# Kernel optimization log

Hardware: AMD Instinct MI355X
Metric: run time of the kernel (lower is better)

The kernel has to match this reference:

```python
import jax, jax.numpy as jnp
import numpy as np

S = 7
BB = 2          # boxes per cell
C = 20          # classes
L_COORD = 5.0
L_NOOBJ = 0.5
L_OBJ = 1.0
L_CLASS = 1.0
BATCH = 8192


def setup_inputs() -> dict:
    key = jax.random.key(0)
    k1, k2, k3, k4 = jax.random.split(key, 4)
    pred = jax.random.normal(k1, (BATCH, S, S, BB * 5 + C), dtype=jnp.float32)
    cls = jax.random.uniform(k2, (BATCH, S, S, C), dtype=jnp.float32)
    # obj conf must be exactly 1.0 where an object exists (obj_mask test is ==1)
    conf = (jax.random.uniform(k3, (BATCH, S, S, 1)) < 0.3).astype(jnp.float32)
    box = jax.random.uniform(k4, (BATCH, S, S, 4), dtype=jnp.float32)  # cx,cy,w,h in [0,1)
    target = jnp.concatenate([cls, conf, box], axis=-1)
    return {"pred": pred, "target": target}


def _iou(a, b):
    # a: (..., BB, 4) cx,cy,w,h ; b: (..., 1, 4)  -> iou (..., BB)
    ax1, ay1 = a[..., 0] - a[..., 2] / 2, a[..., 1] - a[..., 3] / 2
    ax2, ay2 = a[..., 0] + a[..., 2] / 2, a[..., 1] + a[..., 3] / 2
    bx1, by1 = b[..., 0] - b[..., 2] / 2, b[..., 1] - b[..., 3] / 2
    bx2, by2 = b[..., 0] + b[..., 2] / 2, b[..., 1] + b[..., 3] / 2
    iw = jnp.clip(jnp.minimum(ax2, bx2) - jnp.maximum(ax1, bx1), 0.0)
    ih = jnp.clip(jnp.minimum(ay2, by2) - jnp.maximum(ay1, by1), 0.0)
    inter = iw * ih
    union = jnp.abs(a[..., 2] * a[..., 3]) + jnp.abs(b[..., 2] * b[..., 3]) - inter
    return inter / (union + 1e-6)


def reference(pred, target):
    # pred: (N,S,S,B*5+C), target: (N,S,S,5+C)
    objf = (target[..., C] == 1.0).astype(pred.dtype)        # (N,S,S)
    noobjf = 1.0 - objf
    pred_boxes = pred[..., C:].reshape(-1, S, S, BB, 5)       # (N,S,S,B,5) [conf,cx,cy,w,h]
    tb = target[..., C:]                                      # (N,S,S,5)

    ious = _iou(pred_boxes[..., 1:], tb[..., None, 1:])       # (N,S,S,B)
    best = jnp.argmax(ious, axis=-1)                          # responsible box index
    iou_best = jnp.max(ious, axis=-1)                         # (N,S,S)
    pb = jnp.take_along_axis(pred_boxes, best[..., None, None], axis=3)[..., 0, :]  # (N,S,S,5)

    center = jnp.sum((tb[..., 1:3] - pb[..., 1:3]) ** 2, axis=-1)
    # pred wh: pow(2).sqrt().sqrt() == sqrt(|wh|)
    wh = jnp.sum((jnp.sqrt(tb[..., 3:]) - jnp.sqrt(jnp.abs(pb[..., 3:]))) ** 2, axis=-1)
    conf_sq = (tb[..., 0] - pb[..., 0]) ** 2
    cls_sq = jnp.sum((pred[..., :C] - target[..., :C]) ** 2, axis=-1)

    loss = jnp.sum(
        objf * (L_COORD * (center + wh) + L_OBJ * conf_sq + L_CLASS * cls_sq)
        + noobjf * L_NOOBJ * conf_sq
    )
    avg_iou = jnp.sum(iou_best * objf) / jnp.maximum(jnp.sum(objf), 1.0)
    return loss, avg_iou
```

## Files before the change

### kernel.cpp

```cpp
#include <hip/hip_runtime.h>

#define S 7
#define BB 2
#define CLS 20
#define NCELLS (8192 * S * S)
#define CPB 64
#define THREADS 64
#define NBLK (NCELLS / CPB)
#define PRED_F 30
#define TGT_F 25

#define PRED_Q (CPB * PRED_F / 4)
#define TGT_Q  (CPB * TGT_F / 4)

__device__ __forceinline__ float iou_fn(float ax, float ay, float aw, float ah,
                                        float bx, float by, float bw, float bh) {
    float ax1 = ax - aw * 0.5f, ay1 = ay - ah * 0.5f;
    float ax2 = ax + aw * 0.5f, ay2 = ay + ah * 0.5f;
    float bx1 = bx - bw * 0.5f, by1 = by - bh * 0.5f;
    float bx2 = bx + bw * 0.5f, by2 = by + bh * 0.5f;
    float iw = fmaxf(fminf(ax2, bx2) - fmaxf(ax1, bx1), 0.0f);
    float ih = fmaxf(fminf(ay2, by2) - fmaxf(ay1, by1), 0.0f);
    float inter = iw * ih;
    float uni = fabsf(aw * ah) + fabsf(bw * bh) - inter;
    return inter / (uni + 1e-6f);
}

__global__ __launch_bounds__(THREADS) void yolo_main(const float* __restrict__ pred,
                                                     const float* __restrict__ tgt,
                                                     float* __restrict__ pl,
                                                     float* __restrict__ pi,
                                                     float* __restrict__ po) {
    __shared__ float lp[CPB * PRED_F];
    __shared__ float lt[CPB * TGT_F];

    const int b = blockIdx.x;
    const int t = threadIdx.x;

    const float4* gp = (const float4*)(pred + (size_t)b * (CPB * PRED_F));
    float4* sp = (float4*)lp;
    #pragma unroll
    for (int i = 0; i < (PRED_Q + THREADS - 1) / THREADS; ++i) {
        int idx = t + i * THREADS;
        if (idx < PRED_Q) sp[idx] = gp[idx];
    }
    const float4* gt = (const float4*)(tgt + (size_t)b * (CPB * TGT_F));
    float4* st = (float4*)lt;
    #pragma unroll
    for (int i = 0; i < (TGT_Q + THREADS - 1) / THREADS; ++i) {
        int idx = t + i * THREADS;
        if (idx < TGT_Q) st[idx] = gt[idx];
    }
    __syncthreads();

    const float* pp = lp + t * PRED_F;
    const float* tp = lt + t * TGT_F;

    float tconf = tp[CLS + 0];
    float tx = tp[CLS + 1], ty = tp[CLS + 2], tw = tp[CLS + 3], th = tp[CLS + 4];

    float iou0 = iou_fn(pp[CLS + 1], pp[CLS + 2], pp[CLS + 3], pp[CLS + 4], tx, ty, tw, th);
    float iou1 = iou_fn(pp[CLS + 6], pp[CLS + 7], pp[CLS + 8], pp[CLS + 9], tx, ty, tw, th);
    int sel = (iou1 > iou0) ? 1 : 0;
    float iou_best = fmaxf(iou0, iou1);

    const float* pb = pp + CLS + sel * 5;
    float dx = tx - pb[1], dy = ty - pb[2];
    float center = dx * dx + dy * dy;
    float dw = sqrtf(tw) - sqrtf(fabsf(pb[3]));
    float dh = sqrtf(th) - sqrtf(fabsf(pb[4]));
    float wh = dw * dw + dh * dh;
    float dc = tconf - pb[0];
    float conf_sq = dc * dc;

    float cls_sq = 0.0f;
    #pragma unroll
    for (int k = 0; k < CLS; ++k) {
        float d = pp[k] - tp[k];
        cls_sq += d * d;
    }

    float objf = (tconf == 1.0f) ? 1.0f : 0.0f;
    float loss = objf * (5.0f * (center + wh) + conf_sq + cls_sq)
               + (1.0f - objf) * 0.5f * conf_sq;
    float iou_o = objf * iou_best;

    #pragma unroll
    for (int off = 32; off > 0; off >>= 1) {
        loss  += __shfl_down(loss,  off, 64);
        iou_o += __shfl_down(iou_o, off, 64);
        objf  += __shfl_down(objf,  off, 64);
    }
    if (t == 0) {
        pl[b] = loss;
        pi[b] = iou_o;
        po[b] = objf;
    }
}

__global__ __launch_bounds__(256) void yolo_fin(const float* __restrict__ pl,
                                                const float* __restrict__ pi,
                                                const float* __restrict__ po,
                                                float* __restrict__ out) {
    __shared__ float red[3][256 / 64];
    float l = 0.f, i = 0.f, o = 0.f;
    for (int k = threadIdx.x; k < NBLK; k += 256) {
        l += pl[k];
        i += pi[k];
        o += po[k];
    }
    #pragma unroll
    for (int off = 32; off > 0; off >>= 1) {
        l += __shfl_down(l, off, 64);
        i += __shfl_down(i, off, 64);
        o += __shfl_down(o, off, 64);
    }
    const int wave = threadIdx.x >> 6, lane = threadIdx.x & 63;
    if (lane == 0) {
        red[0][wave] = l;
        red[1][wave] = i;
        red[2][wave] = o;
    }
    __syncthreads();
    if (threadIdx.x == 0) {
        float L = 0.f, I = 0.f, O = 0.f;
        #pragma unroll
        for (int w = 0; w < 4; ++w) {
            L += red[0][w];
            I += red[1][w];
            O += red[2][w];
        }
        out[0] = L;
        out[1] = I / fmaxf(O, 1.0f);
    }
}

extern "C" void kernel_launch(void* const* d_in, const int* in_sizes, int n_in,
                              void* d_out, int out_size, void* d_ws, size_t ws_size,
                              hipStream_t stream) {
    const float* pred = (const float*)d_in[0];
    const float* tgt  = (const float*)d_in[1];
    float* out = (float*)d_out;

    float* pl = (float*)d_ws;
    float* pi = pl + NBLK;
    float* po = pi + NBLK;

    yolo_main<<<NBLK, THREADS, 0, stream>>>(pred, tgt, pl, pi, po);
    yolo_fin<<<1, 256, 0, stream>>>(pl, pi, po, out);
}
```

Baseline: 125.9 us.

## Stage tiles via direct global-to-LDS loads and pack per-block partials as float4

Replaces the register-staged float4 copies into shared memory with the global_load_lds builtin (16-byte direct-to-LDS loads), so loaded data skips the VGPRs. Per-block partial sums are written as one float4 instead of three separate arrays. The final reduction runs with 1024 threads reading the float4 partials. This depends on the 16-byte global_load_lds form being supported on the target and on the LDS destination addressing matching the per-lane layout. There is also no explicit wait on the async loads before the barrier.

```diff
diff --git a/kernel.cpp b/kernel.cpp
--- a/kernel.cpp
+++ b/kernel.cpp
@@ -1,4 +1,5 @@
 #include <hip/hip_runtime.h>
+#include <stdint.h>
 
 #define S 7
 #define BB 2
@@ -10,8 +11,10 @@
 #define PRED_F 30
 #define TGT_F 25
 
-#define PRED_Q (CPB * PRED_F / 4)
-#define TGT_Q  (CPB * TGT_F / 4)
+#define ASYNC_CP16(gsrc, ldst)                                                  \
+    __builtin_amdgcn_global_load_lds(                                           \
+        (const __attribute__((address_space(1))) void*)(gsrc),                  \
+        (__attribute__((address_space(3))) void*)(ldst), 16, 0, 0)
 
 __device__ __forceinline__ float iou_fn(float ax, float ay, float aw, float ah,
                                         float bx, float by, float bw, float bh) {
@@ -28,28 +31,28 @@
 
 __global__ __launch_bounds__(THREADS) void yolo_main(const float* __restrict__ pred,
                                                      const float* __restrict__ tgt,
-                                                     float* __restrict__ pl,
-                                                     float* __restrict__ pi,
-                                                     float* __restrict__ po) {
+                                                     float4* __restrict__ part) {
     __shared__ float lp[CPB * PRED_F];
     __shared__ float lt[CPB * TGT_F];
 
     const int b = blockIdx.x;
     const int t = threadIdx.x;
 
-    const float4* gp = (const float4*)(pred + (size_t)b * (CPB * PRED_F));
-    float4* sp = (float4*)lp;
+    const float* gp = pred + (size_t)b * (CPB * PRED_F) + t * 4;
     #pragma unroll
-    for (int i = 0; i < (PRED_Q + THREADS - 1) / THREADS; ++i) {
-        int idx = t + i * THREADS;
-        if (idx < PRED_Q) sp[idx] = gp[idx];
+    for (int i = 0; i < 7; ++i) {
+        ASYNC_CP16(gp + i * 256, lp + i * 256);
     }
-    const float4* gt = (const float4*)(tgt + (size_t)b * (CPB * TGT_F));
-    float4* st = (float4*)lt;
+    if (t < 32) {
+        ASYNC_CP16(gp + 7 * 256, lp + 7 * 256);
+    }
+    const float* gt = tgt + (size_t)b * (CPB * TGT_F) + t * 4;
     #pragma unroll
-    for (int i = 0; i < (TGT_Q + THREADS - 1) / THREADS; ++i) {
-        int idx = t + i * THREADS;
-        if (idx < TGT_Q) st[idx] = gt[idx];
+    for (int i = 0; i < 6; ++i) {
+        ASYNC_CP16(gt + i * 256, lt + i * 256);
+    }
+    if (t < 16) {
+        ASYNC_CP16(gt + 6 * 256, lt + 6 * 256);
     }
     __syncthreads();
 
@@ -92,22 +95,19 @@
         objf  += __shfl_down(objf,  off, 64);
     }
     if (t == 0) {
-        pl[b] = loss;
-        pi[b] = iou_o;
-        po[b] = objf;
+        part[b] = make_float4(loss, iou_o, objf, 0.0f);
     }
 }
 
-__global__ __launch_bounds__(256) void yolo_fin(const float* __restrict__ pl,
-                                                const float* __restrict__ pi,
-                                                const float* __restrict__ po,
-                                                float* __restrict__ out) {
-    __shared__ float red[3][256 / 64];
+__global__ __launch_bounds__(1024) void yolo_fin(const float4* __restrict__ part,
+                                                 float* __restrict__ out) {
+    __shared__ float red[3][1024 / 64];
     float l = 0.f, i = 0.f, o = 0.f;
-    for (int k = threadIdx.x; k < NBLK; k += 256) {
-        l += pl[k];
-        i += pi[k];
-        o += po[k];
+    for (int k = threadIdx.x; k < NBLK; k += 1024) {
+        float4 v = part[k];
+        l += v.x;
+        i += v.y;
+        o += v.z;
     }
     #pragma unroll
     for (int off = 32; off > 0; off >>= 1) {
@@ -125,7 +125,7 @@
     if (threadIdx.x == 0) {
         float L = 0.f, I = 0.f, O = 0.f;
         #pragma unroll
-        for (int w = 0; w < 4; ++w) {
+        for (int w = 0; w < 1024 / 64; ++w) {
             L += red[0][w];
             I += red[1][w];
             O += red[2][w];
@@ -141,11 +141,8 @@
     const float* pred = (const float*)d_in[0];
     const float* tgt  = (const float*)d_in[1];
     float* out = (float*)d_out;
+    float4* part = (float4*)d_ws;
 
-    float* pl = (float*)d_ws;
-    float* pi = pl + NBLK;
-    float* po = pi + NBLK;
-
-    yolo_main<<<NBLK, THREADS, 0, stream>>>(pred, tgt, pl, pi, po);
-    yolo_fin<<<1, 256, 0, stream>>>(pl, pi, po, out);
+    yolo_main<<<NBLK, THREADS, 0, stream>>>(pred, tgt, part);
+    yolo_fin<<<1, 1024, 0, stream>>>(part, out);
 }
```

New measurement: 105.3 us (median of 2 runs). 16.3% less time.
